# Performance work log

Hardware: AMD Instinct MI355X
Metric: run time of the kernel (lower is better)

## Reference

```python
import jax, jax.numpy as jnp
import numpy as np


def _squash_global(v):
    # Faithful to torch: v.norm() with no dim -> global Frobenius norm (scalar).
    n2 = jnp.sum(v * v)
    n = jnp.sqrt(n2)
    scale = n2 / (1.0 + n2)
    return scale * v / n


def setup_inputs() -> dict:
    key = jax.random.key(0)
    k1, k2 = jax.random.split(key)
    B, R, Ci = 128, 1152, 8
    C, O = 10, 16
    x = jax.random.normal(k1, (B, R, Ci), dtype=jnp.float32)
    W = jax.random.normal(k2, (C, R, Ci, O), dtype=jnp.float32)  # routing_weights ~ randn
    return {"x": x, "W": W, "num_iterations": 3}


def reference(x, W, num_iterations):
    # prediction_vectors: [C, B, R, 1, O]
    u = jnp.einsum('bri,crio->cbro', x, W)[:, :, :, None, :]
    logits = jnp.zeros_like(u)
    v = None
    for _ in range(num_iterations):
        # batch_softmax: cat over dim0 + legacy softmax(dim=1 of 4D) == softmax over
        # the num_route_nodes axis (axis 2 here).
        c = jax.nn.softmax(logits, axis=2)
        s = jnp.sum(c * u, axis=2, keepdims=True)  # [C, B, 1, 1, O]
        v = _squash_global(s)
        logits = logits + u * v
    return v
```

## Files before the change

kernel.cpp:

```cpp
#include <hip/hip_runtime.h>
#include <math.h>

#define Bn   128
#define Rn   1152
#define CIn  8
#define Cn   10
#define On   16
#define BO   2048
#define CBO  20480
#define RC   12
#define NSEG 96
#define PSEG 24

__global__ __launch_bounds__(256)
void transpose_x(const float* __restrict__ X, float* __restrict__ XT)
{
    const int r = blockIdx.x;
    const int b = threadIdx.x & 127;
    const int g = threadIdx.x >> 7;
    float4 v = *(const float4*)(X + (size_t)b * (Rn * CIn) + r * CIn + g * 4);
    ((float4*)XT)[r * 256 + g * 128 + b] = v;
}

template<int PASS>
__global__ __launch_bounds__(512, 4)
void pass_kernel(const float* __restrict__ XT, const float* __restrict__ W,
                 const float* __restrict__ Sprev, const float* __restrict__ N2,
                 float* __restrict__ PT, float* __restrict__ PL)
{
    __shared__ float red[8][64][18];

    const int blk  = blockIdx.x;
    const int c    = blk / 48;
    const int rem  = blk - c * 48;
    const int bh   = rem / 24;
    const int segq = rem - bh * 24;
    const int tid  = threadIdx.x;
    const int w    = tid >> 6;
    const int lane = tid & 63;
    const int b    = bh * 64 + lane;
    const int oh   = w >> 2;
    const int sw   = w & 3;
    const int r0   = __builtin_amdgcn_readfirstlane((segq * 4 + sw) * RC);
    const int ohs  = __builtin_amdgcn_readfirstlane(oh * 8);

    float vs[8];
    if (PASS > 1) {
        float coef[PASS];
        #pragma unroll
        for (int t = 0; t < PASS - 1; ++t) {
            const float n2 = N2[t];
            coef[t] = n2 / ((1.0f + n2) * sqrtf(n2)) * 1.4426950408889634f;
        }
        const float* sp = Sprev + c * BO + b * On + ohs;
        #pragma unroll
        for (int q = 0; q < 2; ++q) {
            float4 a = make_float4(0.f, 0.f, 0.f, 0.f);
            #pragma unroll
            for (int t = 0; t < PASS - 1; ++t) {
                const float4 s4 = *(const float4*)(sp + t * CBO + q * 4);
                a.x = fmaf(coef[t], s4.x, a.x);
                a.y = fmaf(coef[t], s4.y, a.y);
                a.z = fmaf(coef[t], s4.z, a.z);
                a.w = fmaf(coef[t], s4.w, a.w);
            }
            vs[q * 4 + 0] = a.x; vs[q * 4 + 1] = a.y;
            vs[q * 4 + 2] = a.z; vs[q * 4 + 3] = a.w;
        }
    }

    float tacc[8], lacc[8];
    #pragma unroll
    for (int o = 0; o < 8; ++o) { tacc[o] = 0.0f; lacc[o] = 0.0f; }

    const float4* XT4 = (const float4*)XT;
    for (int rr = 0; rr < RC; ++rr) {
        const int r = r0 + rr;
        const float4 xa = XT4[r * 256 + b];
        const float4 xb = XT4[r * 256 + 128 + b];
        const int woff = __builtin_amdgcn_readfirstlane((c * Rn + r) * 128 + ohs);
        const float* wr = W + woff;
        #pragma unroll
        for (int o = 0; o < 8; ++o) {
            float u = xa.x * wr[o];
            u = fmaf(xa.y, wr[16 + o], u);
            u = fmaf(xa.z, wr[32 + o], u);
            u = fmaf(xa.w, wr[48 + o], u);
            u = fmaf(xb.x, wr[64 + o], u);
            u = fmaf(xb.y, wr[80 + o], u);
            u = fmaf(xb.z, wr[96 + o], u);
            u = fmaf(xb.w, wr[112 + o], u);
            if (PASS == 1) {
                tacc[o] += u;
            } else {
                const float e = exp2f(u * vs[o]);
                lacc[o] += e;
                tacc[o] = fmaf(e, u, tacc[o]);
            }
        }
    }

    #pragma unroll
    for (int o = 0; o < 8; ++o) {
        red[w][lane][o]     = tacc[o];
        red[w][lane][8 + o] = lacc[o];
    }
    __syncthreads();

    {
        const int oh2  = tid >> 8;
        const int rem2 = tid & 255;
        const int bl   = rem2 >> 2;
        const int oq   = rem2 & 3;
        const int bg   = bh * 64 + bl;
        float2 tv, lv;
        float* tp = (float*)&tv;
        float* lp = (float*)&lv;
        #pragma unroll
        for (int q = 0; q < 2; ++q) {
            const int o = oq * 2 + q;
            tp[q] = red[oh2 * 4 + 0][bl][o] + red[oh2 * 4 + 1][bl][o] +
                    red[oh2 * 4 + 2][bl][o] + red[oh2 * 4 + 3][bl][o];
            lp[q] = red[oh2 * 4 + 0][bl][8 + o] + red[oh2 * 4 + 1][bl][8 + o] +
                    red[oh2 * 4 + 2][bl][8 + o] + red[oh2 * 4 + 3][bl][8 + o];
        }
        const int idx = segq * CBO + c * BO + bg * On + oh2 * 8 + oq * 2;
        *(float2*)(PT + idx) = tv;
        if (PASS > 1) *(float2*)(PL + idx) = lv;
    }
}

template<int PASS>
__global__ __launch_bounds__(256)
void combine_kernel(const float* __restrict__ PT, const float* __restrict__ PL,
                    float* __restrict__ Sout, float* __restrict__ n2out)
{
    const int i = blockIdx.x * 256 + threadIdx.x;
    float T = 0.0f, L = 0.0f;
    #pragma unroll
    for (int s = 0; s < PSEG; ++s) T += PT[s * CBO + i];
    if (PASS == 1) {
        L = (float)Rn;
    } else {
        #pragma unroll
        for (int s = 0; s < PSEG; ++s) L += PL[s * CBO + i];
    }
    const float sv = T / L;
    Sout[i] = sv;
    float sq = sv * sv;
    #pragma unroll
    for (int d = 1; d < 64; d <<= 1) sq += __shfl_xor(sq, d);
    __shared__ float red[4];
    if ((threadIdx.x & 63) == 0) red[threadIdx.x >> 6] = sq;
    __syncthreads();
    if (threadIdx.x == 0)
        atomicAdd(n2out, red[0] + red[1] + red[2] + red[3]);
}

__global__ __launch_bounds__(256)
void final_kernel(const float* __restrict__ S, const float* __restrict__ n2p,
                  float* __restrict__ out)
{
    const int i = blockIdx.x * 256 + threadIdx.x;
    const float n2 = *n2p;
    const float coef = n2 / ((1.0f + n2) * sqrtf(n2));
    out[i] = coef * S[i];
}

extern "C" void kernel_launch(void* const* d_in, const int* in_sizes, int n_in,
                              void* d_out, int out_size, void* d_ws, size_t ws_size,
                              hipStream_t stream)
{
    const float* X = (const float*)d_in[0];
    const float* W = (const float*)d_in[1];
    float* ws = (float*)d_ws;
    float* XT = ws;
    float* N2 = XT + Rn * Bn * CIn;
    float* PT = N2 + 4;
    float* PL = PT + PSEG * CBO;
    float* S  = PL + PSEG * CBO;

    hipMemsetAsync(N2, 0, 16, stream);

    transpose_x<<<Rn, 256, 0, stream>>>(X, XT);
    pass_kernel<1><<<480, 512, 0, stream>>>(XT, W, S, N2, PT, PL);
    combine_kernel<1><<<80, 256, 0, stream>>>(PT, PL, S + 0 * CBO, N2 + 0);
    pass_kernel<2><<<480, 512, 0, stream>>>(XT, W, S, N2, PT, PL);
    combine_kernel<2><<<80, 256, 0, stream>>>(PT, PL, S + 1 * CBO, N2 + 1);
    pass_kernel<3><<<480, 512, 0, stream>>>(XT, W, S, N2, PT, PL);
    combine_kernel<3><<<80, 256, 0, stream>>>(PT, PL, S + 2 * CBO, N2 + 2);
    final_kernel<<<80, 256, 0, stream>>>(S + 2 * CBO, N2 + 2, (float*)d_out);
}
```

Measured before the change: 122.6 us.

## Stage W tile in LDS, halve rows per block, prefetch next x row

Each block now cooperatively loads its 24-row slice of W into shared memory and reads it with float4 LDS loads, instead of scalar uniform global loads per output. The grid doubles to 960 blocks with 6 rows per wave, and the next x row is prefetched in registers to hide global latency. The added cost is a second partial-sum segment count (48), which doubles the partial buffer traffic in the combine kernels, plus an extra barrier and LDS reuse between the W tile and the reduction buffer.

```diff
diff --git a/kernel.cpp b/kernel.cpp
--- a/kernel.cpp
+++ b/kernel.cpp
@@ -8,9 +8,11 @@
 #define On   16
 #define BO   2048
 #define CBO  20480
-#define RC   12
-#define NSEG 96
-#define PSEG 24
+#define RC   6
+#define PSEG 48
+#define GRID 960
+#define NTHR 512
+
 
 __global__ __launch_bounds__(256)
 void transpose_x(const float* __restrict__ X, float* __restrict__ XT)
@@ -23,26 +25,34 @@
 }
 
 template<int PASS>
-__global__ __launch_bounds__(512, 4)
+__global__ __launch_bounds__(NTHR, 4)
 void pass_kernel(const float* __restrict__ XT, const float* __restrict__ W,
                  const float* __restrict__ Sprev, const float* __restrict__ N2,
                  float* __restrict__ PT, float* __restrict__ PL)
 {
-    __shared__ float red[8][64][18];
+    __shared__ __align__(16) float smem[8 * 64 * 18];
+    float (*wlds)[128]   = (float (*)[128])smem;
+    float (*red)[64][18] = (float (*)[64][18])smem;
 
     const int blk  = blockIdx.x;
-    const int c    = blk / 48;
-    const int rem  = blk - c * 48;
-    const int bh   = rem / 24;
-    const int segq = rem - bh * 24;
+    const int c    = blk / 96;
+    const int rem  = blk - c * 96;
+    const int bh   = rem / 48;
+    const int segq = rem - bh * 48;
     const int tid  = threadIdx.x;
     const int w    = tid >> 6;
     const int lane = tid & 63;
     const int b    = bh * 64 + lane;
     const int oh   = w >> 2;
     const int sw   = w & 3;
-    const int r0   = __builtin_amdgcn_readfirstlane((segq * 4 + sw) * RC);
     const int ohs  = __builtin_amdgcn_readfirstlane(oh * 8);
+
+    {
+        const float4* gw4 = (const float4*)(W + (size_t)(c * Rn + segq * 24) * 128);
+        float4* sw4 = (float4*)smem;
+        sw4[tid] = gw4[tid];
+        if (tid < 256) sw4[512 + tid] = gw4[512 + tid];
+    }
 
     float vs[8];
     if (PASS > 1) {
@@ -73,37 +83,51 @@
     #pragma unroll
     for (int o = 0; o < 8; ++o) { tacc[o] = 0.0f; lacc[o] = 0.0f; }
 
+    __syncthreads();
+
     const float4* XT4 = (const float4*)XT;
+    const float4* xp  = XT4 + (size_t)(segq * 24 + sw * RC) * 256 + b;
+    float4 xa = xp[0];
+    float4 xb = xp[128];
     for (int rr = 0; rr < RC; ++rr) {
-        const int r = r0 + rr;
-        const float4 xa = XT4[r * 256 + b];
-        const float4 xb = XT4[r * 256 + 128 + b];
-        const int woff = __builtin_amdgcn_readfirstlane((c * Rn + r) * 128 + ohs);
-        const float* wr = W + woff;
+        const int nx = (rr + 1 < RC) ? (rr + 1) : rr;
+        const float4 nxa = xp[nx * 256];
+        const float4 nxb = xp[nx * 256 + 128];
+        const int lrow = sw * RC + rr;
+        const float xi[8] = { xa.x, xa.y, xa.z, xa.w, xb.x, xb.y, xb.z, xb.w };
+
+        float u[8];
+        #pragma unroll
+        for (int o = 0; o < 8; ++o) u[o] = 0.0f;
+        #pragma unroll
+        for (int i = 0; i < 8; ++i) {
+            const float4 w0 = *(const float4*)&wlds[lrow][i * 16 + ohs + 0];
+            const float4 w1 = *(const float4*)&wlds[lrow][i * 16 + ohs + 4];
+            const float x = xi[i];
+            u[0] = fmaf(x, w0.x, u[0]);  u[1] = fmaf(x, w0.y, u[1]);
+            u[2] = fmaf(x, w0.z, u[2]);  u[3] = fmaf(x, w0.w, u[3]);
+            u[4] = fmaf(x, w1.x, u[4]);  u[5] = fmaf(x, w1.y, u[5]);
+            u[6] = fmaf(x, w1.z, u[6]);  u[7] = fmaf(x, w1.w, u[7]);
+        }
         #pragma unroll
         for (int o = 0; o < 8; ++o) {
-            float u = xa.x * wr[o];
-            u = fmaf(xa.y, wr[16 + o], u);
-            u = fmaf(xa.z, wr[32 + o], u);
-            u = fmaf(xa.w, wr[48 + o], u);
-            u = fmaf(xb.x, wr[64 + o], u);
-            u = fmaf(xb.y, wr[80 + o], u);
-            u = fmaf(xb.z, wr[96 + o], u);
-            u = fmaf(xb.w, wr[112 + o], u);
             if (PASS == 1) {
-                tacc[o] += u;
+                tacc[o] += u[o];
             } else {
-                const float e = exp2f(u * vs[o]);
+                const float e = exp2f(u[o] * vs[o]);
                 lacc[o] += e;
-                tacc[o] = fmaf(e, u, tacc[o]);
+                tacc[o] = fmaf(e, u[o], tacc[o]);
             }
         }
-    }
+        xa = nxa; xb = nxb;
+    }
+
+    __syncthreads();
 
     #pragma unroll
     for (int o = 0; o < 8; ++o) {
-        red[w][lane][o]     = tacc[o];
-        red[w][lane][8 + o] = lacc[o];
+        red[w][lane][o] = tacc[o];
+        if (PASS > 1) red[w][lane][8 + o] = lacc[o];
     }
     __syncthreads();
 
@@ -119,10 +143,10 @@
         #pragma unroll
         for (int q = 0; q < 2; ++q) {
             const int o = oq * 2 + q;
-            tp[q] = red[oh2 * 4 + 0][bl][o] + red[oh2 * 4 + 1][bl][o] +
-                    red[oh2 * 4 + 2][bl][o] + red[oh2 * 4 + 3][bl][o];
-            lp[q] = red[oh2 * 4 + 0][bl][8 + o] + red[oh2 * 4 + 1][bl][8 + o] +
-                    red[oh2 * 4 + 2][bl][8 + o] + red[oh2 * 4 + 3][bl][8 + o];
+            tp[q] = red[oh2*4+0][bl][o] + red[oh2*4+1][bl][o] +
+                    red[oh2*4+2][bl][o] + red[oh2*4+3][bl][o];
+            lp[q] = red[oh2*4+0][bl][8+o] + red[oh2*4+1][bl][8+o] +
+                    red[oh2*4+2][bl][8+o] + red[oh2*4+3][bl][8+o];
         }
         const int idx = segq * CBO + c * BO + bg * On + oh2 * 8 + oq * 2;
         *(float2*)(PT + idx) = tv;
@@ -137,12 +161,12 @@
 {
     const int i = blockIdx.x * 256 + threadIdx.x;
     float T = 0.0f, L = 0.0f;
-    #pragma unroll
+    #pragma unroll 8
     for (int s = 0; s < PSEG; ++s) T += PT[s * CBO + i];
     if (PASS == 1) {
         L = (float)Rn;
     } else {
-        #pragma unroll
+        #pragma unroll 8
         for (int s = 0; s < PSEG; ++s) L += PL[s * CBO + i];
     }
     const float sv = T / L;
@@ -183,11 +207,11 @@
     hipMemsetAsync(N2, 0, 16, stream);
 
     transpose_x<<<Rn, 256, 0, stream>>>(X, XT);
-    pass_kernel<1><<<480, 512, 0, stream>>>(XT, W, S, N2, PT, PL);
+    pass_kernel<1><<<GRID, NTHR, 0, stream>>>(XT, W, S, N2, PT, PL);
     combine_kernel<1><<<80, 256, 0, stream>>>(PT, PL, S + 0 * CBO, N2 + 0);
-    pass_kernel<2><<<480, 512, 0, stream>>>(XT, W, S, N2, PT, PL);
+    pass_kernel<2><<<GRID, NTHR, 0, stream>>>(XT, W, S, N2, PT, PL);
     combine_kernel<2><<<80, 256, 0, stream>>>(PT, PL, S + 1 * CBO, N2 + 1);
-    pass_kernel<3><<<480, 512, 0, stream>>>(XT, W, S, N2, PT, PL);
+    pass_kernel<3><<<GRID, NTHR, 0, stream>>>(XT, W, S, N2, PT, PL);
     combine_kernel<3><<<80, 256, 0, stream>>>(PT, PL, S + 2 * CBO, N2 + 2);
     final_kernel<<<80, 256, 0, stream>>>(S + 2 * CBO, N2 + 2, (float*)d_out);
 }
```

Result: slower. 136.3 us (+11.2%).
